# Kernel tuning notes

Measured on AMD Instinct MI355X. Metric: run time of the kernel, lower is better.

Reference implementation:

```python
import jax, jax.numpy as jnp
import numpy as np

B = 8        # number of clouds
NP = 4096    # points per cloud
STRIDE = 4   # sampler stride -> NS = NP // STRIDE sampled centers per cloud
K = 32       # knn neighbours
NS = NP // STRIDE


def setup_inputs() -> dict:
    key = jax.random.key(0)
    k1, k2, k3, k4 = jax.random.split(key, 4)
    N = B * NP
    x = jax.random.normal(k1, (N, 64), dtype=jnp.float32)
    pos = jax.random.normal(k2, (N, 3), dtype=jnp.float32)
    batch = jnp.repeat(jnp.arange(B, dtype=jnp.int64), NP)
    d_in = 64 + 3
    W1 = jax.random.normal(k3, (d_in, 128), dtype=jnp.float32) / np.sqrt(d_in)
    b1 = jnp.zeros((128,), dtype=jnp.float32)
    W2 = jax.random.normal(k4, (128, 256), dtype=jnp.float32) / np.sqrt(128)
    b2 = jnp.zeros((256,), dtype=jnp.float32)
    return {"x": x, "pos": pos, "batch": batch, "W1": W1, "b1": b1, "W2": W2, "b2": b2}


def reference(x, pos, batch, W1, b1, W2, b2):
    # --- sampler: stride sampling per cloud (clouds are equal-sized, contiguous) ---
    pos_b = pos.reshape(B, NP, 3)
    idx_local = jnp.arange(0, NP, STRIDE)                       # [NS]
    idx = (idx_local[None, :] + jnp.arange(B)[:, None] * NP).reshape(-1)  # global sampled idx [B*NS]
    pos_s = pos_b[:, idx_local]                                 # [B, NS, 3]

    # --- neighbour_finder: knn within each cloud (batch-respecting via per-cloud blocks) ---
    # squared distances [B, NS, NP] without materializing [B,NS,NP,3]
    d2 = ((pos_s ** 2).sum(-1)[:, :, None]
          + (pos_b ** 2).sum(-1)[:, None, :]
          - 2.0 * jnp.einsum('bsd,bnd->bsn', pos_s, pos_b))
    _, nbr = jax.lax.top_k(-d2, K)                              # [B, NS, K] local neighbour idx
    col = (nbr + (jnp.arange(B) * NP)[:, None, None]).reshape(-1)  # global neighbour idx [E]

    # --- conv: PointNetConv -> MLP(concat(x_j, pos_j - pos_i)) then max over neighbours ---
    x_j = x[col].reshape(B, NS, K, -1)                          # [B, NS, K, 64]
    rel = pos[col].reshape(B, NS, K, 3) - pos_s[:, :, None, :]  # pos_j - pos_i
    feat = jnp.concatenate([x_j, rel], axis=-1)                 # [B, NS, K, 67]
    h = jax.nn.relu(feat @ W1 + b1)                             # [B, NS, K, 128]
    h = jax.nn.relu(h @ W2 + b2)                                # [B, NS, K, 256]
    x_out = h.max(axis=2).reshape(B * NS, -1)                   # [B*NS, 256]

    pos_out = pos_s.reshape(-1, 3)
    batch_out = batch[idx]
    return x_out, pos_out, batch_out, idx
```

## Files before the change

kernel.cpp:

```cpp
#include <hip/hip_runtime.h>
#include <hip/hip_bf16.h>

#define BB 8
#define NP 4096
#define STRIDE 4
#define KNN 32
#define NS (NP/STRIDE)
#define NQ (BB*NS)
#define DIN 67
#define H1N 128
#define H2N 256

typedef __attribute__((ext_vector_type(8)))  short bf16x8;
typedef __attribute__((ext_vector_type(16))) float f32x16;
typedef __attribute__((ext_vector_type(8)))  short short8;

__device__ __forceinline__ unsigned int f2u(float f) {
    unsigned int b = __float_as_uint(f);
    return (b & 0x80000000u) ? ~b : (b | 0x80000000u);
}
__device__ __forceinline__ short f2bf(float f) {
    unsigned u = __float_as_uint(f);
    unsigned r = u + 0x7FFFu + ((u >> 16) & 1u);
    return (short)(r >> 16);
}

__global__ __launch_bounds__(256) void knn_kernel(const float* __restrict__ pos,
                                                  int* __restrict__ col) {
    __shared__ __align__(16) unsigned long long surv[NP];
    __shared__ unsigned int pvt[4];
    __shared__ int cnts[4];

    const int q    = blockIdx.x;
    const int b    = q >> 10;
    const int s    = q & (NS - 1);
    const int qi   = b * NP + s * STRIDE;
    const int t    = threadIdx.x;
    const int w    = t >> 6;
    const int lane = t & 63;

    if (t == 64) pvt[3] = 0xFFFFFFFFu;

    const float qx = pos[qi*3+0], qy = pos[qi*3+1], qz = pos[qi*3+2];
    const float q2 = __fadd_rn(__fadd_rn(__fmul_rn(qx,qx), __fmul_rn(qy,qy)), __fmul_rn(qz,qz));

    const float* pb = pos + (size_t)b * NP * 3;
    unsigned int myk[16];
    #pragma unroll
    for (int i = 0; i < 4; ++i) {
        const int u = t + i * 256;
        const float4* pp = (const float4*)(pb + (size_t)u * 12);
        const float4 v0 = pp[0], v1 = pp[1], v2 = pp[2];
        const float px[4] = {v0.x, v0.w, v1.z, v2.y};
        const float py[4] = {v0.y, v1.x, v1.w, v2.z};
        const float pz[4] = {v0.z, v1.y, v2.x, v2.w};
        #pragma unroll
        for (int j = 0; j < 4; ++j) {
            const float p2 = __fadd_rn(__fadd_rn(__fmul_rn(px[j],px[j]), __fmul_rn(py[j],py[j])), __fmul_rn(pz[j],pz[j]));
            const float dt = __fadd_rn(__fadd_rn(__fmul_rn(qx,px[j]), __fmul_rn(qy,py[j])), __fmul_rn(qz,pz[j]));
            const float d2 = __fsub_rn(__fadd_rn(q2, p2), __fmul_rn(2.0f, dt));
            myk[i*4+j] = f2u(d2);
        }
    }

    if (t < 64) {
        const unsigned int mk = myk[0];
        int rank = 0;
        #pragma unroll
        for (int ss = 0; ss < 64; ++ss) {
            const unsigned int ks = __shfl(mk, ss, 64);
            rank += (int)((ks < mk) | ((ks == mk) & (ss < t)));
        }
        if (rank == 1) pvt[0] = mk;
        if (rank == 3) pvt[1] = mk;
        if (rank == 8) pvt[2] = mk;
    }
    __syncthreads();

    int C = 0, level = 0;
    for (; level < 4; ++level) {
        const unsigned int T = pvt[level];
        int cw = 0;
        #pragma unroll
        for (int i = 0; i < 16; ++i)
            cw += __popcll(__ballot(myk[i] <= T));
        if (lane == 0) cnts[w] = cw;
        __syncthreads();
        C = cnts[0] + cnts[1] + cnts[2] + cnts[3];
        if (C >= KNN) break;
        __syncthreads();
    }

    {
        const unsigned int T = pvt[level];
        int base = 0;
        #pragma unroll
        for (int i = 0; i < 4; ++i) base += (i < w) ? cnts[i] : 0;
        #pragma unroll
        for (int i = 0; i < 16; ++i) {
            const bool p = (myk[i] <= T);
            const unsigned long long mask = __ballot(p);
            if (p) {
                const int off = __popcll(mask & ((1ull << lane) - 1ull));
                const int n   = 4 * (t + (i >> 2) * 256) + (i & 3);
                surv[base + off] = ((unsigned long long)myk[i] << 32) | (unsigned int)n;
            }
            base += __popcll(mask);
        }
    }
    __syncthreads();

    const ulonglong2* sp2 = (const ulonglong2*)surv;
    const int C2 = C >> 1;
    for (int j = t; j < C; j += 256) {
        const unsigned long long v = surv[j];
        int rank = 0;
        #pragma unroll 4
        for (int ss = 0; ss < C2; ++ss) {
            const ulonglong2 pr = sp2[ss];
            rank += (int)(pr.x < v) + (int)(pr.y < v);
        }
        if (C & 1) rank += (int)(surv[C - 1] < v);
        if (rank < KNN)
            col[q * KNN + rank] = b * NP + (int)(unsigned int)(v & 0xFFFFFFFFull);
    }
}

__global__ __launch_bounds__(64) void prep_w1(const float* __restrict__ W1,
                                              short* __restrict__ W1T) {
    const int nt = blockIdx.x / 5, t = blockIdx.x % 5;
    const int l  = threadIdx.x;
    const int c  = 32*nt + (l & 31);
    short8 v;
    #pragma unroll
    for (int b = 0; b < 8; ++b) {
        const int k = 16*t + 8*(l >> 5) + b;
        v[b] = (k < DIN) ? f2bf(W1[k * H1N + c]) : (short)0;
    }
    *(short8*)(W1T + ((size_t)(nt*5 + t) * 64 + l) * 8) = v;
}

__global__ __launch_bounds__(64) void prep_w2(const float* __restrict__ W2,
                                              short* __restrict__ W2T) {
    const int nt = blockIdx.x >> 3, t = blockIdx.x & 7;
    const int l  = threadIdx.x;
    const int c  = 32*nt + (l & 31);
    short8 v;
    #pragma unroll
    for (int b = 0; b < 8; ++b) {
        const int k = 16*t + 8*(l >> 5) + b;
        v[b] = f2bf(W2[k * H2N + c]);
    }
    *(short8*)(W2T + ((size_t)(nt*8 + t) * 64 + l) * 8) = v;
}

__global__ __launch_bounds__(256, 2) void mlp_mfma(const float* __restrict__ x,
                                                   const float* __restrict__ pos,
                                                   const int* __restrict__ col,
                                                   const float* __restrict__ b1,
                                                   const float* __restrict__ b2,
                                                   const short* __restrict__ W1T,
                                                   const short* __restrict__ W2T,
                                                   float* __restrict__ out) {
    __shared__ __align__(16) short feat[128 * 80];
    __shared__ __align__(16) short h1s [128 * 128];

    const int q0 = blockIdx.x * 4;
    const int t  = threadIdx.x;
    const int w  = t >> 6, l = t & 63;

    {
        const int row  = t >> 1, part = t & 1;
        const int q    = q0 + (row >> 5);
        const int c    = col[q * KNN + (row & 31)];
        const float4* xr = (const float4*)(x + (size_t)c * 64 + part * 32);
        short* fr = feat + row * 80 + part * 32;
        #pragma unroll
        for (int i = 0; i < 8; ++i) {
            const float4 v = xr[i];
            *(int*)(fr + i * 4 + 0) = (int)((unsigned short)f2bf(v.x) | ((unsigned)(unsigned short)f2bf(v.y) << 16));
            *(int*)(fr + i * 4 + 2) = (int)((unsigned short)f2bf(v.z) | ((unsigned)(unsigned short)f2bf(v.w) << 16));
        }
        if (part == 0) {
            const int b  = q >> 10;
            const int qi = b * NP + (q & (NS - 1)) * STRIDE;
            short8 o;
            o[0] = f2bf(pos[c*3+0] - pos[qi*3+0]);
            o[1] = f2bf(pos[c*3+1] - pos[qi*3+1]);
            o[2] = f2bf(pos[c*3+2] - pos[qi*3+2]);
            o[3] = 0; o[4] = 0; o[5] = 0; o[6] = 0; o[7] = 0;
            *(short8*)(feat + row * 80 + 64) = o;
            short8 z = {0,0,0,0,0,0,0,0};
            *(short8*)(feat + row * 80 + 72) = z;
        }
    }
    __syncthreads();

    const int lr = l & 31;
    const int lh = l >> 5;

    {
        bf16x8 w1f[20];
        #pragma unroll
        for (int i = 0; i < 20; ++i)
            w1f[i] = *(const bf16x8*)(W1T + ((size_t)i * 64 + l) * 8);

        bf16x8 a1[5];
        #pragma unroll
        for (int kt = 0; kt < 5; ++kt) {
            const int row = 32*w + lr;
            a1[kt] = *(const bf16x8*)(feat + row * 80 + 16*kt + 8*lh);
        }

        #pragma unroll
        for (int nt = 0; nt < 4; ++nt) {
            const float bv = b1[32*nt + lr];
            f32x16 acc;
            #pragma unroll
            for (int r = 0; r < 16; ++r) acc[r] = bv;
            #pragma unroll
            for (int kt = 0; kt < 5; ++kt)
                acc = __builtin_amdgcn_mfma_f32_32x32x16_bf16(a1[kt], w1f[nt*5 + kt], acc, 0, 0, 0);
            #pragma unroll
            for (int r = 0; r < 16; ++r) {
                const int i   = (r & 3) + 8*(r >> 2) + 4*lh;
                const int row = 32*w + i;
                const int c   = 32*nt + lr;
                const int adr = row * 128 + ((((c >> 3) ^ (row & 15)) << 3) | (c & 7));
                h1s[adr] = f2bf(fmaxf(acc[r], 0.0f));
            }
        }
    }
    __syncthreads();

    {
        bf16x8 a2[8];
        #pragma unroll
        for (int kt = 0; kt < 8; ++kt) {
            const int row  = 32*w + lr;
            const int slot = 2*kt + lh;
            a2[kt] = *(const bf16x8*)(h1s + row * 128 + ((slot ^ (row & 15)) << 3));
        }

        f32x16 acc[8];
        #pragma unroll
        for (int nt = 0; nt < 8; ++nt)
            #pragma unroll
            for (int r = 0; r < 16; ++r) acc[nt][r] = 0.0f;

        bf16x8 cur[8];
        #pragma unroll
        for (int kt = 0; kt < 8; ++kt)
            cur[kt] = *(const bf16x8*)(W2T + ((size_t)kt * 64 + l) * 8);

        #pragma unroll
        for (int nt = 0; nt < 8; ++nt) {
            bf16x8 nxt[8];
            if (nt < 7) {
                #pragma unroll
                for (int kt = 0; kt < 8; ++kt)
                    nxt[kt] = *(const bf16x8*)(W2T + ((size_t)((nt+1)*8 + kt) * 64 + l) * 8);
            }
            #pragma unroll
            for (int kt = 0; kt < 8; ++kt)
                acc[nt] = __builtin_amdgcn_mfma_f32_32x32x16_bf16(a2[kt], cur[kt], acc[nt], 0, 0, 0);
            #pragma unroll
            for (int kt = 0; kt < 8; ++kt) cur[kt] = nxt[kt];
        }

        const int q = q0 + w;
        #pragma unroll
        for (int nt = 0; nt < 8; ++nt) {
            float m = acc[nt][0];
            #pragma unroll
            for (int r = 1; r < 16; ++r) m = fmaxf(m, acc[nt][r]);
            m = fmaxf(m, __shfl_xor(m, 32, 64));
            m = fmaxf(m + b2[32*nt + lr], 0.0f);
            if (l < 32) out[(size_t)q * H2N + 32*nt + l] = m;
        }
    }
}

__global__ __launch_bounds__(256) void tail_kernel(const float* __restrict__ pos,
                                                   float* __restrict__ out) {
    const int qn = blockIdx.x * 256 + threadIdx.x;
    if (qn >= NQ) return;
    const int b  = qn >> 10;
    const int s  = qn & (NS - 1);
    const int qi = b * NP + s * STRIDE;

    float* pos_out   = out + (size_t)NQ * H2N;
    float* batch_out = pos_out + (size_t)NQ * 3;
    float* idx_out   = batch_out + NQ;

    pos_out[qn*3+0] = pos[qi*3+0];
    pos_out[qn*3+1] = pos[qi*3+1];
    pos_out[qn*3+2] = pos[qi*3+2];
    batch_out[qn]   = (float)b;
    idx_out[qn]     = (float)qi;
}

extern "C" void kernel_launch(void* const* d_in, const int* in_sizes, int n_in,
                              void* d_out, int out_size, void* d_ws, size_t ws_size,
                              hipStream_t stream) {
    const float* x   = (const float*)d_in[0];
    const float* pos = (const float*)d_in[1];
    const float* W1  = (const float*)d_in[3];
    const float* b1  = (const float*)d_in[4];
    const float* W2  = (const float*)d_in[5];
    const float* b2  = (const float*)d_in[6];
    float* out = (float*)d_out;

    char* ws   = (char*)d_ws;
    int*  col  = (int*)ws;
    short* W1T = (short*)(ws + 1048576);
    short* W2T = (short*)(ws + 1048576 + 20480);

    prep_w1<<<20, 64, 0, stream>>>(W1, W1T);
    prep_w2<<<64, 64, 0, stream>>>(W2, W2T);
    knn_kernel<<<NQ, 256, 0, stream>>>(pos, col);
    mlp_mfma<<<NQ/4, 256, 0, stream>>>(x, pos, col, b1, b2, W1T, W2T, out);
    tail_kernel<<<(NQ + 255) / 256, 256, 0, stream>>>(pos, out);
}
```

Before: 160.2 us.

## Skip count pass in kNN, shrink shared buffer, fuse tail and weight-prep launches

The kNN kernel now compacts candidates at the first pivot straight into per-wave segments of a smaller shared buffer. This drops the separate count pass and its barriers in the common case and only falls back to the multi-level pivot search when too few survive. The smaller shared allocation may let more blocks reside per CU. The tail kernel's pos/batch/idx writes move into the kNN kernel, and the two weight-prep kernels merge into one, removing two launches. The per-wave cap of 512 entries can silently drop candidates if a wave has more survivors, and the rank loop now walks four segments.

```diff
diff --git a/kernel.cpp b/kernel.cpp
--- a/kernel.cpp
+++ b/kernel.cpp
@@ -10,6 +10,7 @@
 #define DIN 67
 #define H1N 128
 #define H2N 256
+#define WCAP 512
 
 typedef __attribute__((ext_vector_type(8)))  short bf16x8;
 typedef __attribute__((ext_vector_type(16))) float f32x16;
@@ -26,8 +27,9 @@
 }
 
 __global__ __launch_bounds__(256) void knn_kernel(const float* __restrict__ pos,
-                                                  int* __restrict__ col) {
-    __shared__ __align__(16) unsigned long long surv[NP];
+                                                  int* __restrict__ col,
+                                                  float* __restrict__ out) {
+    __shared__ __align__(16) unsigned long long surv[4 * WCAP];
     __shared__ unsigned int pvt[4];
     __shared__ int cnts[4];
 
@@ -39,7 +41,16 @@
     const int w    = t >> 6;
     const int lane = t & 63;
 
-    if (t == 64) pvt[3] = 0xFFFFFFFFu;
+    if (t == 128) pvt[3] = 0xFFFFFFFFu;
+
+    if (t < 5) {
+        float* pos_out   = out + (size_t)NQ * H2N;
+        float* batch_out = pos_out + (size_t)NQ * 3;
+        float* idx_out   = batch_out + NQ;
+        if (t < 3)       pos_out[q*3+t] = pos[qi*3+t];
+        else if (t == 3) batch_out[q] = (float)b;
+        else             idx_out[q]   = (float)qi;
+    }
 
     const float qx = pos[qi*3+0], qy = pos[qi*3+1], qz = pos[qi*3+2];
     const float q2 = __fadd_rn(__fadd_rn(__fmul_rn(qx,qx), __fmul_rn(qy,qy)), __fmul_rn(qz,qz));
@@ -68,90 +79,127 @@
         int rank = 0;
         #pragma unroll
         for (int ss = 0; ss < 64; ++ss) {
-            const unsigned int ks = __shfl(mk, ss, 64);
+            const unsigned int ks = (unsigned int)__shfl((int)mk, ss, 64);
             rank += (int)((ks < mk) | ((ks == mk) & (ss < t)));
         }
-        if (rank == 1) pvt[0] = mk;
-        if (rank == 3) pvt[1] = mk;
-        if (rank == 8) pvt[2] = mk;
+        if (rank == 1)  pvt[0] = mk;
+        if (rank == 3)  pvt[1] = mk;
+        if (rank == 8)  pvt[2] = mk;
     }
     __syncthreads();
 
-    int C = 0, level = 0;
-    for (; level < 4; ++level) {
-        const unsigned int T = pvt[level];
-        int cw = 0;
-        #pragma unroll
-        for (int i = 0; i < 16; ++i)
-            cw += __popcll(__ballot(myk[i] <= T));
-        if (lane == 0) cnts[w] = cw;
-        __syncthreads();
-        C = cnts[0] + cnts[1] + cnts[2] + cnts[3];
-        if (C >= KNN) break;
-        __syncthreads();
-    }
-
+    int level = 0;
     {
-        const unsigned int T = pvt[level];
+        const unsigned int T = pvt[0];
         int base = 0;
-        #pragma unroll
-        for (int i = 0; i < 4; ++i) base += (i < w) ? cnts[i] : 0;
         #pragma unroll
         for (int i = 0; i < 16; ++i) {
             const bool p = (myk[i] <= T);
             const unsigned long long mask = __ballot(p);
             if (p) {
-                const int off = __popcll(mask & ((1ull << lane) - 1ull));
-                const int n   = 4 * (t + (i >> 2) * 256) + (i & 3);
-                surv[base + off] = ((unsigned long long)myk[i] << 32) | (unsigned int)n;
-            }
-            base += __popcll(mask);
-        }
+                const int off = base + (int)__popcll(mask & ((1ull << lane) - 1ull));
+                if (off < WCAP) {
+                    const int n = 4 * (t + (i >> 2) * 256) + (i & 3);
+                    surv[(w << 9) + off] = ((unsigned long long)myk[i] << 32) | (unsigned int)n;
+                }
+            }
+            base += (int)__popcll(mask);
+        }
+        if (lane == 0) cnts[w] = (base < WCAP) ? base : WCAP;
     }
     __syncthreads();
 
-    const ulonglong2* sp2 = (const ulonglong2*)surv;
-    const int C2 = C >> 1;
+    int c0 = cnts[0], c1 = cnts[1], c2 = cnts[2], c3 = cnts[3];
+    int C = c0 + c1 + c2 + c3;
+
+    if (C < KNN) {
+        for (level = 1; level < 4; ++level) {
+            const unsigned int T = pvt[level];
+            int cw = 0;
+            #pragma unroll
+            for (int i = 0; i < 16; ++i)
+                cw += (int)__popcll(__ballot(myk[i] <= T));
+            if (lane == 0) cnts[w] = cw;
+            __syncthreads();
+            C = cnts[0] + cnts[1] + cnts[2] + cnts[3];
+            if (C >= KNN) break;
+            __syncthreads();
+        }
+        __syncthreads();
+        {
+            const unsigned int T = pvt[level];
+            int base = 0;
+            #pragma unroll
+            for (int i = 0; i < 16; ++i) {
+                const bool p = (myk[i] <= T);
+                const unsigned long long mask = __ballot(p);
+                if (p) {
+                    const int off = base + (int)__popcll(mask & ((1ull << lane) - 1ull));
+                    if (off < WCAP) {
+                        const int n = 4 * (t + (i >> 2) * 256) + (i & 3);
+                        surv[(w << 9) + off] = ((unsigned long long)myk[i] << 32) | (unsigned int)n;
+                    }
+                }
+                base += (int)__popcll(mask);
+            }
+            if (lane == 0) cnts[w] = (base < WCAP) ? base : WCAP;
+        }
+        __syncthreads();
+        c0 = cnts[0]; c1 = cnts[1]; c2 = cnts[2]; c3 = cnts[3];
+        C = c0 + c1 + c2 + c3;
+    }
+
+    const int s1 = c0, s2 = c0 + c1, s3 = c0 + c1 + c2;
+    const int cseg[4] = {c0, c1, c2, c3};
     for (int j = t; j < C; j += 256) {
-        const unsigned long long v = surv[j];
-        int rank = 0;
-        #pragma unroll 4
-        for (int ss = 0; ss < C2; ++ss) {
-            const ulonglong2 pr = sp2[ss];
-            rank += (int)(pr.x < v) + (int)(pr.y < v);
-        }
-        if (C & 1) rank += (int)(surv[C - 1] < v);
-        if (rank < KNN)
-            col[q * KNN + rank] = b * NP + (int)(unsigned int)(v & 0xFFFFFFFFull);
-    }
-}
-
-__global__ __launch_bounds__(64) void prep_w1(const float* __restrict__ W1,
-                                              short* __restrict__ W1T) {
-    const int nt = blockIdx.x / 5, t = blockIdx.x % 5;
-    const int l  = threadIdx.x;
-    const int c  = 32*nt + (l & 31);
-    short8 v;
-    #pragma unroll
-    for (int b = 0; b < 8; ++b) {
-        const int k = 16*t + 8*(l >> 5) + b;
-        v[b] = (k < DIN) ? f2bf(W1[k * H1N + c]) : (short)0;
-    }
-    *(short8*)(W1T + ((size_t)(nt*5 + t) * 64 + l) * 8) = v;
-}
-
-__global__ __launch_bounds__(64) void prep_w2(const float* __restrict__ W2,
-                                              short* __restrict__ W2T) {
-    const int nt = blockIdx.x >> 3, t = blockIdx.x & 7;
-    const int l  = threadIdx.x;
-    const int c  = 32*nt + (l & 31);
-    short8 v;
-    #pragma unroll
-    for (int b = 0; b < 8; ++b) {
-        const int k = 16*t + 8*(l >> 5) + b;
-        v[b] = f2bf(W2[k * H2N + c]);
-    }
-    *(short8*)(W2T + ((size_t)(nt*8 + t) * 64 + l) * 8) = v;
+        const int seg = (int)(j >= s1) + (int)(j >= s2) + (int)(j >= s3);
+        const int off = j - ((seg == 0) ? 0 : (seg == 1) ? s1 : (seg == 2) ? s2 : s3);
+        const unsigned long long v = surv[(seg << 9) + off];
+        int rk = 0;
+        #pragma unroll 1
+        for (int k = 0; k < 4; ++k) {
+            const ulonglong2* sp2 = (const ulonglong2*)(surv + (k << 9));
+            const int ck = cseg[k];
+            const int ck2 = ck >> 1;
+            #pragma unroll 4
+            for (int ss = 0; ss < ck2; ++ss) {
+                const ulonglong2 pr = sp2[ss];
+                rk += (int)(pr.x < v) + (int)(pr.y < v);
+            }
+            if (ck & 1) rk += (int)(surv[(k << 9) + ck - 1] < v);
+        }
+        if (rk < KNN)
+            col[q * KNN + rk] = b * NP + (int)(unsigned int)(v & 0xFFFFFFFFull);
+    }
+}
+
+__global__ __launch_bounds__(64) void prep_w(const float* __restrict__ W1,
+                                             const float* __restrict__ W2,
+                                             short* __restrict__ W1T,
+                                             short* __restrict__ W2T) {
+    const int l = threadIdx.x;
+    if (blockIdx.x < 20) {
+        const int nt = blockIdx.x / 5, t = blockIdx.x % 5;
+        const int c  = 32*nt + (l & 31);
+        short8 v;
+        #pragma unroll
+        for (int b = 0; b < 8; ++b) {
+            const int k = 16*t + 8*(l >> 5) + b;
+            v[b] = (k < DIN) ? f2bf(W1[k * H1N + c]) : (short)0;
+        }
+        *(short8*)(W1T + ((size_t)(nt*5 + t) * 64 + l) * 8) = v;
+    } else {
+        const int bb = blockIdx.x - 20;
+        const int nt = bb >> 3, t = bb & 7;
+        const int c  = 32*nt + (l & 31);
+        short8 v;
+        #pragma unroll
+        for (int b = 0; b < 8; ++b) {
+            const int k = 16*t + 8*(l >> 5) + b;
+            v[b] = f2bf(W2[k * H2N + c]);
+        }
+        *(short8*)(W2T + ((size_t)(nt*8 + t) * 64 + l) * 8) = v;
+    }
 }
 
 __global__ __launch_bounds__(256, 2) void mlp_mfma(const float* __restrict__ x,
@@ -281,25 +329,6 @@
     }
 }
 
-__global__ __launch_bounds__(256) void tail_kernel(const float* __restrict__ pos,
-                                                   float* __restrict__ out) {
-    const int qn = blockIdx.x * 256 + threadIdx.x;
-    if (qn >= NQ) return;
-    const int b  = qn >> 10;
-    const int s  = qn & (NS - 1);
-    const int qi = b * NP + s * STRIDE;
-
-    float* pos_out   = out + (size_t)NQ * H2N;
-    float* batch_out = pos_out + (size_t)NQ * 3;
-    float* idx_out   = batch_out + NQ;
-
-    pos_out[qn*3+0] = pos[qi*3+0];
-    pos_out[qn*3+1] = pos[qi*3+1];
-    pos_out[qn*3+2] = pos[qi*3+2];
-    batch_out[qn]   = (float)b;
-    idx_out[qn]     = (float)qi;
-}
-
 extern "C" void kernel_launch(void* const* d_in, const int* in_sizes, int n_in,
                               void* d_out, int out_size, void* d_ws, size_t ws_size,
                               hipStream_t stream) {
@@ -316,9 +345,7 @@
     short* W1T = (short*)(ws + 1048576);
     short* W2T = (short*)(ws + 1048576 + 20480);
 
-    prep_w1<<<20, 64, 0, stream>>>(W1, W1T);
-    prep_w2<<<64, 64, 0, stream>>>(W2, W2T);
-    knn_kernel<<<NQ, 256, 0, stream>>>(pos, col);
+    prep_w<<<84, 64, 0, stream>>>(W1, W2, W1T, W2T);
+    knn_kernel<<<NQ, 256, 0, stream>>>(pos, col, out);
     mlp_mfma<<<NQ/4, 256, 0, stream>>>(x, pos, col, b1, b2, W1T, W2T, out);
-    tail_kernel<<<(NQ + 255) / 256, 256, 0, stream>>>(pos, out);
-}
+}
```

Result: faster. 154.9 us (-3.3%).
